# Optimization experiments

Measured on AMD Instinct MI355X. Metric: run time of the kernel, lower is better.

## Reference

```python
import jax, jax.numpy as jnp
import numpy as np

TIME = 10  # interpolation factor, hardcoded in the torch module


def _interpolation(poly, time=TIME):
    # poly: [B, M, 2] -> [B, M*time, 2]
    poly_roll = jnp.roll(poly, shift=1, axis=1)
    step = jnp.arange(time, dtype=poly.dtype) / time  # [time]
    # interp[b, m, t, c] = poly[b,m,c]*step[t] + roll[b,m,c]*(1-step[t])
    interp = (poly[:, :, None, :] * step[None, None, :, None]
              + poly_roll[:, :, None, :] * (1.0 - step)[None, None, :, None])
    B, M = poly.shape[0], poly.shape[1]
    return interp.reshape(B, M * time, 2)


def _compute_distance(pred_poly, gt_poly):
    # pred: [B, N, 2], gt: [B, G, 2] -> sq dist [B, G, N]
    diff = pred_poly[:, None, :, :] - gt_poly[:, :, None, :]
    return jnp.sum(diff * diff, axis=3)


def setup_inputs() -> dict:
    key = jax.random.key(0)
    k1, k2, k3 = jax.random.split(key, 3)
    B, N, M = 1024, 128, 128
    return {
        "ini_pred_poly": jax.random.normal(k1, (B, N, 2), dtype=jnp.float32),
        "pred_polys_": jax.random.normal(k2, (B, N, 2), dtype=jnp.float32),
        "gt_polys": jax.random.normal(k3, (B, M, 2), dtype=jnp.float32),
        "keyPointsMask": jnp.ones((B, M), dtype=jnp.float32),
    }


def reference(ini_pred_poly, pred_polys_, gt_polys, keyPointsMask):
    # ---- lossPred2NearestGt ----
    gt_interp = _interpolation(gt_polys)                     # [B, M*T, 2]
    dist_pg = _compute_distance(ini_pred_poly, gt_interp)    # [B, M*T, N]
    index_gt = jnp.argmin(dist_pg, axis=1)                   # [B, N]
    nearest_gt = jnp.take_along_axis(gt_interp, index_gt[:, :, None], axis=1)  # [B, N, 2]
    loss_pred2gt = jnp.mean(jnp.abs(pred_polys_ - nearest_gt))  # l1, mean reduction

    # ---- lossGt2NearestPred ----
    dist_gp = _compute_distance(ini_pred_poly, gt_polys)     # [B, M, N]
    index_pred = jnp.argmin(dist_gp, axis=2)                 # [B, M]
    nearest_pred = jnp.take_along_axis(pred_polys_, index_pred[:, :, None], axis=1)  # [B, M, 2]
    loss_gt2pred = jnp.abs(nearest_pred - gt_polys)          # [B, M, 2], reduction='none'

    mask = keyPointsMask[:, :, None] * jnp.ones((1, 1, 2), dtype=keyPointsMask.dtype)  # [B, M, 2]
    loss_set2set = jnp.sum(loss_gt2pred * mask) / (jnp.sum(mask) + 1.0) + loss_pred2gt
    return loss_set2set / 2.0
```

## Files before the change

kernel.cpp:

```cpp
#include <hip/hip_runtime.h>

constexpr int Bn = 1024;
constexpr int Mn = 128;


__global__ __launch_bounds__(256) void dm_pre(
    const float2* __restrict__ ini,
    const float2* __restrict__ gt,
    float4* __restrict__ seg)
{
    const int idx = blockIdx.x * 256 + threadIdx.x;
    const int b = idx >> 7, m = idx & 127;
    const float2 cur = gt[idx];
    const float2 prv = gt[(b << 7) | ((m + 127) & 127)];
    const float2 ii  = ini[idx];
    const float ex = cur.x - prv.x, ey = cur.y - prv.y;
    const float ee = fmaxf(fmaf(ex, ex, ey * ey), 1e-30f);
    const float nr = -10.0f * __builtin_amdgcn_rcpf(ee);
    seg[2*idx]     = make_float4(prv.x, prv.y, ex, ey);
    seg[2*idx + 1] = make_float4(ee, nr, ii.x, ii.y);
}

__global__ __launch_bounds__(512) void dm_main(
    const float2* __restrict__ ini,
    const float2* __restrict__ pred,
    const float2* __restrict__ gt,
    const float*  __restrict__ kpm,
    const float4* __restrict__ seg,
    float4* __restrict__ part)
{
    __shared__ unsigned sA[4][Mn];
    __shared__ unsigned sB[4][Mn];
    __shared__ float    s_red[3][8];

    const int b   = blockIdx.x;
    const int tid = threadIdx.x;
    const int p   = tid & 127;
    const int q   = __builtin_amdgcn_readfirstlane(tid >> 7);
    const int base = b * (2 * Mn);

    const float2 P = ini[b*Mn + p];
    const float2 g = gt [b*Mn + p];

    unsigned bestA = 0xFFFFFFFFu, bestB = 0xFFFFFFFFu;
    #pragma unroll 8
    for (int i = 0; i < 32; ++i) {
        const int m = q*32 + i;
        const float4 A1 = seg[base + 2*m];
        const float4 A2 = seg[base + 2*m + 1];
        const float fx = A1.x - P.x, fy = A1.y - P.y;
        const float fe = fmaf(fx, A1.z, fy*A1.w);
        const float ff = fmaf(fx, fx, fy*fy);
        const float sp = 0.1f * __builtin_amdgcn_fmed3f(rintf(fe*A2.y), 0.f, 9.f);
        const float d  = fmaxf(fmaf(sp, fmaf(sp, A2.x, fe + fe), ff), 0.f);
        bestA = min(bestA, (__float_as_uint(d) & 0xFFFFFF80u) | (unsigned)m);
        const float dx = A2.z - g.x, dy = A2.w - g.y;
        const float d2 = fmaf(dx, dx, dy*dy);
        bestB = min(bestB, (__float_as_uint(d2) & 0xFFFFFF80u) | (unsigned)m);
    }
    sA[q][p] = bestA;
    sB[q][p] = bestB;
    __syncthreads();

    float sum_p2g = 0.f, sum_g2p = 0.f, sum_m = 0.f;
    if (tid < Mn) {
        bestA = min(min(sA[0][p], sA[1][p]), min(sA[2][p], sA[3][p]));
        bestB = min(min(sB[0][p], sB[1][p]), min(sB[2][p], sB[3][p]));

        const int bm = bestA & 127;
        const float4 R1 = seg[base + 2*bm];
        const float4 R2 = seg[base + 2*bm + 1];
        const float fx = R1.x - P.x, fy = R1.y - P.y;
        const float fe = fmaf(fx, R1.z, fy*R1.w);
        const float sp = 0.1f * __builtin_amdgcn_fmed3f(rintf(fe*R2.y), 0.f, 9.f);
        const float ngx = fmaf(sp, R1.z, R1.x);
        const float ngy = fmaf(sp, R1.w, R1.y);
        const float2 pr = pred[b*Mn + p];
        sum_p2g = fabsf(pr.x - ngx) + fabsf(pr.y - ngy);

        const int   ni_ = bestB & 127;
        const float2 np_ = pred[b*Mn + ni_];
        const float  w   = kpm[b*Mn + p];
        sum_g2p = w * (fabsf(np_.x - g.x) + fabsf(np_.y - g.y));
        sum_m   = 2.0f * w;
    }

    #pragma unroll
    for (int off = 32; off > 0; off >>= 1) {
        sum_p2g += __shfl_down(sum_p2g, off);
        sum_g2p += __shfl_down(sum_g2p, off);
        sum_m   += __shfl_down(sum_m,   off);
    }
    const int wv = tid >> 6;
    if ((tid & 63) == 0) { s_red[0][wv] = sum_p2g; s_red[1][wv] = sum_g2p; s_red[2][wv] = sum_m; }
    __syncthreads();
    if (tid == 0) {
        part[b] = make_float4(s_red[0][0] + s_red[0][1],
                              s_red[1][0] + s_red[1][1],
                              s_red[2][0] + s_red[2][1], 0.f);
    }
}

__global__ __launch_bounds__(1024) void dm_final(const float4* __restrict__ part,
                                                 float* __restrict__ out)
{
    __shared__ float s_red[3][16];
    const int tid = threadIdx.x;
    const float4 v = part[tid];
    float a = v.x, c = v.y, m = v.z;
    #pragma unroll
    for (int off = 32; off > 0; off >>= 1) {
        a += __shfl_down(a, off); c += __shfl_down(c, off); m += __shfl_down(m, off);
    }
    const int wv = tid >> 6;
    if ((tid & 63) == 0) { s_red[0][wv] = a; s_red[1][wv] = c; s_red[2][wv] = m; }
    __syncthreads();
    if (tid == 0) {
        float A = 0.f, C = 0.f, M = 0.f;
        #pragma unroll
        for (int i = 0; i < 16; ++i) { A += s_red[0][i]; C += s_red[1][i]; M += s_red[2][i]; }
        out[0] = (C / (M + 1.0f) + A * (1.0f / 262144.0f)) * 0.5f;
    }
}

extern "C" void kernel_launch(void* const* d_in, const int* in_sizes, int n_in,
                              void* d_out, int out_size, void* d_ws, size_t ws_size,
                              hipStream_t stream)
{
    const float2* ini  = (const float2*)d_in[0];
    const float2* pred = (const float2*)d_in[1];
    const float2* gt   = (const float2*)d_in[2];
    const float*  kpm  = (const float*)d_in[3];
    float* out = (float*)d_out;

    float4* seg  = (float4*)d_ws;
    float4* part = seg + Bn * Mn * 2;

    dm_pre <<<Bn * Mn / 256, 256, 0, stream>>>(ini, gt, seg);
    dm_main<<<Bn, 512, 0, stream>>>(ini, pred, gt, kpm, seg, part);
    dm_final<<<1, 1024, 0, stream>>>(part, out);
}
```

Measured before the change: 74.93 us.

## Fuse precompute, main and final reduction into one single-pass kernel

Merges the segment precompute, the per-batch argmin kernel and the final reduction into one kernel. Each block stages gt and ini points in shared memory and recomputes segment terms (including a reciprocal) inline instead of reading a precomputed global buffer. Two threads per point split the candidates and combine with a lane shuffle. The final scalar is produced with global atomics and a last-block counter after a memset, which removes two launches and a global round trip but adds per-iteration ALU work and makes the float sum order nondeterministic.

```diff
diff --git a/kernel.cpp b/kernel.cpp
--- a/kernel.cpp
+++ b/kernel.cpp
@@ -4,84 +4,79 @@
 constexpr int Mn = 128;
 
 
-__global__ __launch_bounds__(256) void dm_pre(
-    const float2* __restrict__ ini,
-    const float2* __restrict__ gt,
-    float4* __restrict__ seg)
-{
-    const int idx = blockIdx.x * 256 + threadIdx.x;
-    const int b = idx >> 7, m = idx & 127;
-    const float2 cur = gt[idx];
-    const float2 prv = gt[(b << 7) | ((m + 127) & 127)];
-    const float2 ii  = ini[idx];
-    const float ex = cur.x - prv.x, ey = cur.y - prv.y;
-    const float ee = fmaxf(fmaf(ex, ex, ey * ey), 1e-30f);
-    const float nr = -10.0f * __builtin_amdgcn_rcpf(ee);
-    seg[2*idx]     = make_float4(prv.x, prv.y, ex, ey);
-    seg[2*idx + 1] = make_float4(ee, nr, ii.x, ii.y);
-}
-
-__global__ __launch_bounds__(512) void dm_main(
+__global__ __launch_bounds__(256) void dm_all(
     const float2* __restrict__ ini,
     const float2* __restrict__ pred,
     const float2* __restrict__ gt,
     const float*  __restrict__ kpm,
-    const float4* __restrict__ seg,
-    float4* __restrict__ part)
+    float* __restrict__ acc,
+    float* __restrict__ out)
 {
-    __shared__ unsigned sA[4][Mn];
-    __shared__ unsigned sB[4][Mn];
-    __shared__ float    s_red[3][8];
+    __shared__ float4 s_pts[Mn];
+    __shared__ float  s_red[3][4];
 
     const int b   = blockIdx.x;
     const int tid = threadIdx.x;
-    const int p   = tid & 127;
-    const int q   = __builtin_amdgcn_readfirstlane(tid >> 7);
-    const int base = b * (2 * Mn);
+    const int p   = tid >> 1;
+    const int q   = tid & 1;
 
-    const float2 P = ini[b*Mn + p];
-    const float2 g = gt [b*Mn + p];
+    if (tid < Mn) {
+        const float2 gv = gt [b*Mn + tid];
+        const float2 iv = ini[b*Mn + tid];
+        s_pts[tid] = make_float4(gv.x, gv.y, iv.x, iv.y);
+    }
+    __syncthreads();
+
+    const float4 me = s_pts[p];
+    const float Px = me.z, Py = me.w;
+    const float gx = me.x, gy = me.y;
+
+    const int m0 = q * 64;
+    float ax, ay;
+    { const float4 t0 = s_pts[(m0 + Mn - 1) & (Mn - 1)]; ax = t0.x; ay = t0.y; }
 
     unsigned bestA = 0xFFFFFFFFu, bestB = 0xFFFFFFFFu;
     #pragma unroll 8
-    for (int i = 0; i < 32; ++i) {
-        const int m = q*32 + i;
-        const float4 A1 = seg[base + 2*m];
-        const float4 A2 = seg[base + 2*m + 1];
-        const float fx = A1.x - P.x, fy = A1.y - P.y;
-        const float fe = fmaf(fx, A1.z, fy*A1.w);
+    for (int i = 0; i < 64; ++i) {
+        const int m = m0 + i;
+        const float4 c = s_pts[m];
+        const float ex = c.x - ax, ey = c.y - ay;
+        const float ee = fmaxf(fmaf(ex, ex, ey*ey), 1e-30f);
+        const float nr = -10.0f * __builtin_amdgcn_rcpf(ee);
+        const float fx = ax - Px, fy = ay - Py;
+        const float fe = fmaf(fx, ex, fy*ey);
         const float ff = fmaf(fx, fx, fy*fy);
-        const float sp = 0.1f * __builtin_amdgcn_fmed3f(rintf(fe*A2.y), 0.f, 9.f);
-        const float d  = fmaxf(fmaf(sp, fmaf(sp, A2.x, fe + fe), ff), 0.f);
+        const float sp = 0.1f * __builtin_amdgcn_fmed3f(rintf(fe*nr), 0.f, 9.f);
+        const float d  = fmaxf(fmaf(sp, fmaf(sp, ee, fe + fe), ff), 0.f);
         bestA = min(bestA, (__float_as_uint(d) & 0xFFFFFF80u) | (unsigned)m);
-        const float dx = A2.z - g.x, dy = A2.w - g.y;
+        const float dx = c.z - gx, dy = c.w - gy;
         const float d2 = fmaf(dx, dx, dy*dy);
         bestB = min(bestB, (__float_as_uint(d2) & 0xFFFFFF80u) | (unsigned)m);
+        ax = c.x; ay = c.y;
     }
-    sA[q][p] = bestA;
-    sB[q][p] = bestB;
-    __syncthreads();
+    bestA = min(bestA, (unsigned)__shfl_xor((int)bestA, 1));
+    bestB = min(bestB, (unsigned)__shfl_xor((int)bestB, 1));
 
     float sum_p2g = 0.f, sum_g2p = 0.f, sum_m = 0.f;
-    if (tid < Mn) {
-        bestA = min(min(sA[0][p], sA[1][p]), min(sA[2][p], sA[3][p]));
-        bestB = min(min(sB[0][p], sB[1][p]), min(sB[2][p], sB[3][p]));
-
+    if (q == 0) {
         const int bm = bestA & 127;
-        const float4 R1 = seg[base + 2*bm];
-        const float4 R2 = seg[base + 2*bm + 1];
-        const float fx = R1.x - P.x, fy = R1.y - P.y;
-        const float fe = fmaf(fx, R1.z, fy*R1.w);
-        const float sp = 0.1f * __builtin_amdgcn_fmed3f(rintf(fe*R2.y), 0.f, 9.f);
-        const float ngx = fmaf(sp, R1.z, R1.x);
-        const float ngy = fmaf(sp, R1.w, R1.y);
+        const float4 cb = s_pts[bm];
+        const float4 cp = s_pts[(bm + Mn - 1) & (Mn - 1)];
+        const float ex = cb.x - cp.x, ey = cb.y - cp.y;
+        const float ee = fmaxf(fmaf(ex, ex, ey*ey), 1e-30f);
+        const float nr = -10.0f * __builtin_amdgcn_rcpf(ee);
+        const float fx = cp.x - Px, fy = cp.y - Py;
+        const float fe = fmaf(fx, ex, fy*ey);
+        const float sp = 0.1f * __builtin_amdgcn_fmed3f(rintf(fe*nr), 0.f, 9.f);
+        const float ngx = fmaf(sp, ex, cp.x);
+        const float ngy = fmaf(sp, ey, cp.y);
         const float2 pr = pred[b*Mn + p];
         sum_p2g = fabsf(pr.x - ngx) + fabsf(pr.y - ngy);
 
         const int   ni_ = bestB & 127;
         const float2 np_ = pred[b*Mn + ni_];
         const float  w   = kpm[b*Mn + p];
-        sum_g2p = w * (fabsf(np_.x - g.x) + fabsf(np_.y - g.y));
+        sum_g2p = w * (fabsf(np_.x - gx) + fabsf(np_.y - gy));
         sum_m   = 2.0f * w;
     }
 
@@ -95,31 +90,17 @@
     if ((tid & 63) == 0) { s_red[0][wv] = sum_p2g; s_red[1][wv] = sum_g2p; s_red[2][wv] = sum_m; }
     __syncthreads();
     if (tid == 0) {
-        part[b] = make_float4(s_red[0][0] + s_red[0][1],
-                              s_red[1][0] + s_red[1][1],
-                              s_red[2][0] + s_red[2][1], 0.f);
-    }
-}
-
-__global__ __launch_bounds__(1024) void dm_final(const float4* __restrict__ part,
-                                                 float* __restrict__ out)
-{
-    __shared__ float s_red[3][16];
-    const int tid = threadIdx.x;
-    const float4 v = part[tid];
-    float a = v.x, c = v.y, m = v.z;
-    #pragma unroll
-    for (int off = 32; off > 0; off >>= 1) {
-        a += __shfl_down(a, off); c += __shfl_down(c, off); m += __shfl_down(m, off);
-    }
-    const int wv = tid >> 6;
-    if ((tid & 63) == 0) { s_red[0][wv] = a; s_red[1][wv] = c; s_red[2][wv] = m; }
-    __syncthreads();
-    if (tid == 0) {
-        float A = 0.f, C = 0.f, M = 0.f;
-        #pragma unroll
-        for (int i = 0; i < 16; ++i) { A += s_red[0][i]; C += s_red[1][i]; M += s_red[2][i]; }
-        out[0] = (C / (M + 1.0f) + A * (1.0f / 262144.0f)) * 0.5f;
+        atomicAdd(&acc[0], s_red[0][0] + s_red[0][1] + s_red[0][2] + s_red[0][3]);
+        atomicAdd(&acc[1], s_red[1][0] + s_red[1][1] + s_red[1][2] + s_red[1][3]);
+        atomicAdd(&acc[2], s_red[2][0] + s_red[2][1] + s_red[2][2] + s_red[2][3]);
+        __threadfence();
+        const unsigned old = atomicAdd((unsigned*)&acc[3], 1u);
+        if (old == (unsigned)(gridDim.x - 1)) {
+            const float A = atomicAdd(&acc[0], 0.f);
+            const float C = atomicAdd(&acc[1], 0.f);
+            const float M = atomicAdd(&acc[2], 0.f);
+            out[0] = (C / (M + 1.0f) + A * (1.0f / 262144.0f)) * 0.5f;
+        }
     }
 }
 
@@ -132,11 +113,8 @@
     const float2* gt   = (const float2*)d_in[2];
     const float*  kpm  = (const float*)d_in[3];
     float* out = (float*)d_out;
+    float* acc = (float*)d_ws;
 
-    float4* seg  = (float4*)d_ws;
-    float4* part = seg + Bn * Mn * 2;
-
-    dm_pre <<<Bn * Mn / 256, 256, 0, stream>>>(ini, gt, seg);
-    dm_main<<<Bn, 512, 0, stream>>>(ini, pred, gt, kpm, seg, part);
-    dm_final<<<1, 1024, 0, stream>>>(part, out);
+    hipMemsetAsync(acc, 0, 16, stream);
+    dm_all<<<Bn, 256, 0, stream>>>(ini, pred, gt, kpm, acc, out);
 }
```

Result: slower. 120.4 us (+60.7%).

## Fuse segment precompute into main kernel via LDS and shuffle-reduce argmin

Applied to the files above, without the earlier changes.

Removes the separate pre-pass kernel that wrote per-segment data to global workspace. Each block now builds the segment table in shared memory, then uses 1024 threads, eight per point, with a strided scan over segments. Partial argmins are combined with xor shuffles instead of an LDS exchange. This saves a launch and a global round-trip, at the cost of larger blocks and an extra barrier.

```diff
diff --git a/kernel.cpp b/kernel.cpp
--- a/kernel.cpp
+++ b/kernel.cpp
@@ -4,84 +4,79 @@
 constexpr int Mn = 128;
 
 
-__global__ __launch_bounds__(256) void dm_pre(
-    const float2* __restrict__ ini,
-    const float2* __restrict__ gt,
-    float4* __restrict__ seg)
-{
-    const int idx = blockIdx.x * 256 + threadIdx.x;
-    const int b = idx >> 7, m = idx & 127;
-    const float2 cur = gt[idx];
-    const float2 prv = gt[(b << 7) | ((m + 127) & 127)];
-    const float2 ii  = ini[idx];
-    const float ex = cur.x - prv.x, ey = cur.y - prv.y;
-    const float ee = fmaxf(fmaf(ex, ex, ey * ey), 1e-30f);
-    const float nr = -10.0f * __builtin_amdgcn_rcpf(ee);
-    seg[2*idx]     = make_float4(prv.x, prv.y, ex, ey);
-    seg[2*idx + 1] = make_float4(ee, nr, ii.x, ii.y);
-}
-
-__global__ __launch_bounds__(512) void dm_main(
+__global__ __launch_bounds__(1024) void dm_main(
     const float2* __restrict__ ini,
     const float2* __restrict__ pred,
     const float2* __restrict__ gt,
     const float*  __restrict__ kpm,
-    const float4* __restrict__ seg,
     float4* __restrict__ part)
 {
-    __shared__ unsigned sA[4][Mn];
-    __shared__ unsigned sB[4][Mn];
-    __shared__ float    s_red[3][8];
+    __shared__ float4 s_A[Mn];
+    __shared__ float4 s_B[Mn];
+    __shared__ float  s_red[3][16];
 
     const int b   = blockIdx.x;
     const int tid = threadIdx.x;
-    const int p   = tid & 127;
-    const int q   = __builtin_amdgcn_readfirstlane(tid >> 7);
-    const int base = b * (2 * Mn);
+    const int p   = tid >> 3;
+    const int q   = tid & 7;
 
-    const float2 P = ini[b*Mn + p];
-    const float2 g = gt [b*Mn + p];
+    if (tid < Mn) {
+        const float2 cur = gt[b*Mn + tid];
+        const float2 prv = gt[b*Mn + ((tid + 127) & 127)];
+        const float2 ii  = ini[b*Mn + tid];
+        const float ex = cur.x - prv.x, ey = cur.y - prv.y;
+        const float ee = fmaxf(fmaf(ex, ex, ey*ey), 1e-30f);
+        const float nr = -10.0f * __builtin_amdgcn_rcpf(ee);
+        s_A[tid] = make_float4(prv.x, prv.y, ex, ey);
+        s_B[tid] = make_float4(ee, nr, ii.x, ii.y);
+    }
+    __syncthreads();
+
+    const float4 mb = s_B[p];
+    const float4 ma = s_A[(p + 1) & 127];
+    const float Px = mb.z, Py = mb.w;
+    const float gx = ma.x, gy = ma.y;
 
     unsigned bestA = 0xFFFFFFFFu, bestB = 0xFFFFFFFFu;
-    #pragma unroll 8
-    for (int i = 0; i < 32; ++i) {
-        const int m = q*32 + i;
-        const float4 A1 = seg[base + 2*m];
-        const float4 A2 = seg[base + 2*m + 1];
-        const float fx = A1.x - P.x, fy = A1.y - P.y;
-        const float fe = fmaf(fx, A1.z, fy*A1.w);
+    #pragma unroll
+    for (int i = 0; i < 16; ++i) {
+        const int m = (i << 3) | q;
+        const float4 A  = s_A[m];
+        const float4 Bv = s_B[m];
+        const float fx = A.x - Px, fy = A.y - Py;
+        const float fe = fmaf(fx, A.z, fy*A.w);
         const float ff = fmaf(fx, fx, fy*fy);
-        const float sp = 0.1f * __builtin_amdgcn_fmed3f(rintf(fe*A2.y), 0.f, 9.f);
-        const float d  = fmaxf(fmaf(sp, fmaf(sp, A2.x, fe + fe), ff), 0.f);
+        const float sp = 0.1f * __builtin_amdgcn_fmed3f(rintf(fe*Bv.y), 0.f, 9.f);
+        const float d  = fmaxf(fmaf(sp, fmaf(sp, Bv.x, fe + fe), ff), 0.f);
         bestA = min(bestA, (__float_as_uint(d) & 0xFFFFFF80u) | (unsigned)m);
-        const float dx = A2.z - g.x, dy = A2.w - g.y;
+        const float dx = Bv.z - gx, dy = Bv.w - gy;
         const float d2 = fmaf(dx, dx, dy*dy);
         bestB = min(bestB, (__float_as_uint(d2) & 0xFFFFFF80u) | (unsigned)m);
     }
-    sA[q][p] = bestA;
-    sB[q][p] = bestB;
-    __syncthreads();
+    bestA = min(bestA, (unsigned)__shfl_xor((int)bestA, 1));
+    bestA = min(bestA, (unsigned)__shfl_xor((int)bestA, 2));
+    bestA = min(bestA, (unsigned)__shfl_xor((int)bestA, 4));
+    bestB = min(bestB, (unsigned)__shfl_xor((int)bestB, 1));
+    bestB = min(bestB, (unsigned)__shfl_xor((int)bestB, 2));
+    bestB = min(bestB, (unsigned)__shfl_xor((int)bestB, 4));
 
     float sum_p2g = 0.f, sum_g2p = 0.f, sum_m = 0.f;
-    if (tid < Mn) {
-        bestA = min(min(sA[0][p], sA[1][p]), min(sA[2][p], sA[3][p]));
-        bestB = min(min(sB[0][p], sB[1][p]), min(sB[2][p], sB[3][p]));
-
+    if (q == 0) {
         const int bm = bestA & 127;
-        const float4 R1 = seg[base + 2*bm];
-        const float4 R2 = seg[base + 2*bm + 1];
-        const float fx = R1.x - P.x, fy = R1.y - P.y;
-        const float fe = fmaf(fx, R1.z, fy*R1.w);
-        const float sp = 0.1f * __builtin_amdgcn_fmed3f(rintf(fe*R2.y), 0.f, 9.f);
-        const float ngx = fmaf(sp, R1.z, R1.x);
-        const float ngy = fmaf(sp, R1.w, R1.y);
+        const float4 RA = s_A[bm];
+        const float4 RB = s_B[bm];
+        const float fx = RA.x - Px, fy = RA.y - Py;
+        const float fe = fmaf(fx, RA.z, fy*RA.w);
+        const float sp = 0.1f * __builtin_amdgcn_fmed3f(rintf(fe*RB.y), 0.f, 9.f);
+        const float ngx = fmaf(sp, RA.z, RA.x);
+        const float ngy = fmaf(sp, RA.w, RA.y);
         const float2 pr = pred[b*Mn + p];
         sum_p2g = fabsf(pr.x - ngx) + fabsf(pr.y - ngy);
 
         const int   ni_ = bestB & 127;
         const float2 np_ = pred[b*Mn + ni_];
         const float  w   = kpm[b*Mn + p];
-        sum_g2p = w * (fabsf(np_.x - g.x) + fabsf(np_.y - g.y));
+        sum_g2p = w * (fabsf(np_.x - gx) + fabsf(np_.y - gy));
         sum_m   = 2.0f * w;
     }
 
@@ -95,9 +90,10 @@
     if ((tid & 63) == 0) { s_red[0][wv] = sum_p2g; s_red[1][wv] = sum_g2p; s_red[2][wv] = sum_m; }
     __syncthreads();
     if (tid == 0) {
-        part[b] = make_float4(s_red[0][0] + s_red[0][1],
-                              s_red[1][0] + s_red[1][1],
-                              s_red[2][0] + s_red[2][1], 0.f);
+        float A = 0.f, C = 0.f, M = 0.f;
+        #pragma unroll
+        for (int i = 0; i < 16; ++i) { A += s_red[0][i]; C += s_red[1][i]; M += s_red[2][i]; }
+        part[b] = make_float4(A, C, M, 0.f);
     }
 }
 
@@ -131,12 +127,9 @@
     const float2* pred = (const float2*)d_in[1];
     const float2* gt   = (const float2*)d_in[2];
     const float*  kpm  = (const float*)d_in[3];
-    float* out = (float*)d_out;
+    float*  out  = (float*)d_out;
+    float4* part = (float4*)d_ws;
 
-    float4* seg  = (float4*)d_ws;
-    float4* part = seg + Bn * Mn * 2;
-
-    dm_pre <<<Bn * Mn / 256, 256, 0, stream>>>(ini, gt, seg);
-    dm_main<<<Bn, 512, 0, stream>>>(ini, pred, gt, kpm, seg, part);
+    dm_main <<<Bn, 1024, 0, stream>>>(ini, pred, gt, kpm, part);
     dm_final<<<1, 1024, 0, stream>>>(part, out);
 }
```

After: 73.93 us. Within noise of the previous version (-1.3%).
